# Performance work log

Measured on AMD Instinct MI355X. Metric: run time of the kernel, lower is better.

The kernel has to match this reference:

```python
import jax, jax.numpy as jnp
import numpy as np

N = 100000       # num nodes
E = 1000000      # num edges
D_IN = 128       # node_input_dim
H = 128          # hidden_dim
D_E = 32         # edge_input_dim
C = 16           # num_classes


def setup_inputs() -> dict:
    key = jax.random.key(0)
    ks = jax.random.split(key, 8)
    x = jax.random.normal(ks[0], (N, D_IN), dtype=jnp.float32)
    edge_index = jax.random.randint(ks[1], (2, E), 0, N)
    edge_attr = jax.random.normal(ks[2], (E, D_E), dtype=jnp.float32)

    def glorot(k, shape):
        fan = shape[0]
        return (jax.random.normal(k, shape, dtype=jnp.float32) / np.sqrt(fan)).astype(jnp.float32)

    W1 = glorot(ks[3], (D_IN, H)); b1 = jnp.zeros((H,), jnp.float32)
    W2 = glorot(ks[4], (H, H));    b2 = jnp.zeros((H,), jnp.float32)
    W3 = glorot(ks[5], (H, H));    b3 = jnp.zeros((H,), jnp.float32)
    W_fc = glorot(ks[6], (D_E + 2 * H, C)); b_fc = jnp.zeros((C,), jnp.float32)
    return {"x": x, "edge_index": edge_index, "edge_attr": edge_attr,
            "W1": W1, "b1": b1, "W2": W2, "b2": b2, "W3": W3, "b3": b3,
            "W_fc": W_fc, "b_fc": b_fc}


def gcn_conv(h_in, W, b, src, dst, dinv):
    """PyG GCNConv: h = D^-1/2 (A+I) D^-1/2 (h_in @ W) + b.
    Self-loop contribution handled analytically as dinv[i]^2 * h[i]."""
    h = h_in @ W                                      # [N, H]
    norm = dinv[src] * dinv[dst]                      # [E]
    msgs = h[src] * norm[:, None]                     # gather + scale, [E, H]
    agg = jax.ops.segment_sum(msgs, dst, num_segments=N)  # scatter-add
    agg = agg + h * (dinv * dinv)[:, None]            # self-loops
    return agg + b


def reference(x, edge_index, edge_attr, W1, b1, W2, b2, W3, b3, W_fc, b_fc):
    src, dst = edge_index[0], edge_index[1]
    # degree with self-loops (edge_weight = 1), as in PyG gcn_norm
    deg = jax.ops.segment_sum(jnp.ones((E,), jnp.float32), dst, num_segments=N) + 1.0
    dinv = jax.lax.rsqrt(deg)

    h = jax.nn.relu(gcn_conv(x, W1, b1, src, dst, dinv))
    # dropout(p=0.3) is identity in eval mode
    h = jax.nn.relu(gcn_conv(h, W2, b2, src, dst, dinv))
    h = jax.nn.relu(gcn_conv(h, W3, b3, src, dst, dinv))

    edge_features = jnp.concatenate([h[src], h[dst], edge_attr], axis=1)  # [E, 2H+D_E]
    edge_output = edge_features @ W_fc + b_fc                             # [E, C]
    return jax.nn.log_softmax(edge_output, axis=1)
```

## Files before the change

kernel.cpp:

```cpp
#include <hip/hip_runtime.h>
#include <hip/hip_bf16.h>

#define D_IN 128
#define HDIM 128
#define D_E  32
#define NC   16
#define SCAN_CHUNK 2048

typedef __attribute__((ext_vector_type(8))) short short8;
typedef __attribute__((ext_vector_type(4))) float float4v;

__device__ inline short f2bs(float f) {
  __hip_bfloat16 h = (__hip_bfloat16)f;
  return *reinterpret_cast<short*>(&h);
}

__device__ inline float bs2f(short s) {
  unsigned int u = ((unsigned int)(unsigned short)s) << 16;
  float f;
  __builtin_memcpy(&f, &u, 4);
  return f;
}


__global__ __launch_bounds__(256) void count_deg(const int* __restrict__ ei, int* __restrict__ deg, int E) {
  int e = blockIdx.x * 256 + threadIdx.x;
  if (e < E) atomicAdd(&deg[ei[E + e]], 1);
}

__global__ __launch_bounds__(256) void scan_blocksums(const int* __restrict__ deg, int* __restrict__ bsum, int n) {
  __shared__ int red[256];
  int t = threadIdx.x;
  int base = blockIdx.x * SCAN_CHUNK + t * 8;
  int s = 0;
#pragma unroll
  for (int j = 0; j < 8; ++j) {
    int i = base + j;
    if (i < n) s += deg[i];
  }
  red[t] = s;
  __syncthreads();
  for (int off = 128; off > 0; off >>= 1) {
    if (t < off) red[t] += red[t + off];
    __syncthreads();
  }
  if (t == 0) bsum[blockIdx.x] = red[0];
}

__global__ __launch_bounds__(256) void scan_offsets(const int* __restrict__ bsum, int* __restrict__ boff, int nb) {
  __shared__ int s[256];
  int t = threadIdx.x;
  int v = (t < nb) ? bsum[t] : 0;
  s[t] = v;
  __syncthreads();
  for (int off = 1; off < 256; off <<= 1) {
    int u = (t >= off) ? s[t - off] : 0;
    __syncthreads();
    s[t] += u;
    __syncthreads();
  }
  if (t < nb) boff[t] = (t == 0) ? 0 : s[t - 1];
}

__global__ __launch_bounds__(256) void scan_write(const int* __restrict__ deg, const int* __restrict__ boff,
                                                  int* __restrict__ rowptr, float* __restrict__ dinv, int n) {
  __shared__ int red[256];
  int t = threadIdx.x;
  int base = blockIdx.x * SCAN_CHUNK + t * 8;
  int v[8];
  int s = 0;
#pragma unroll
  for (int j = 0; j < 8; ++j) {
    int i = base + j;
    v[j] = (i < n) ? deg[i] : 0;
    s += v[j];
  }
  red[t] = s;
  __syncthreads();
  for (int off = 1; off < 256; off <<= 1) {
    int u = (t >= off) ? red[t - off] : 0;
    __syncthreads();
    red[t] += u;
    __syncthreads();
  }
  int run = red[t] - s + boff[blockIdx.x];
#pragma unroll
  for (int j = 0; j < 8; ++j) {
    int i = base + j;
    if (i < n) {
      rowptr[i] = run;
      dinv[i] = rsqrtf((float)v[j] + 1.0f);
    }
    run += v[j];
  }
}

__global__ __launch_bounds__(256) void fill_csr(const int* __restrict__ ei, const int* __restrict__ rowptr,
                                                int* __restrict__ cursor, int* __restrict__ col, int E) {
  int e = blockIdx.x * 256 + threadIdx.x;
  if (e < E) {
    int d = ei[E + e];
    int pos = atomicAdd(&cursor[d], 1);
    col[rowptr[d] + pos] = ei[e];
  }
}

__global__ __launch_bounds__(256) void repack_w128(const float* __restrict__ W, short* __restrict__ wp) {
  int idx = blockIdx.x * 256 + threadIdx.x;
  if (idx < 16384) {
    int j = idx & 7, lane = (idx >> 3) & 63, t = (idx >> 9) & 7, kc = idx >> 12;
    int k = kc * 32 + (lane >> 4) * 8 + j;
    int nn = t * 16 + (lane & 15);
    wp[idx] = f2bs(W[k * HDIM + nn]);
  }
}

__global__ __launch_bounds__(256) void repack_wcp(const float* __restrict__ Wfc, short* __restrict__ wp) {
  int idx = blockIdx.x * 256 + threadIdx.x;
  if (idx < 4096) {
    int j = idx & 7, lane = (idx >> 3) & 63, t = (idx >> 9) & 1, kc = idx >> 10;
    int k = kc * 32 + (lane >> 4) * 8 + j;
    int nn = t * 16 + (lane & 15);
    float v = (nn < 16) ? Wfc[k * NC + nn] : Wfc[(HDIM + k) * NC + (nn - 16)];
    wp[idx] = f2bs(v);
  }
}

template<int NCOL, bool FP32IN, bool FP32OUT, bool SCALE>
__global__ __launch_bounds__(256) void gemm_mfma(const void* __restrict__ Xv, const short* __restrict__ wpack,
                                                 void* __restrict__ Yv, const float* __restrict__ dscale, int n) {
  constexpr int NT = NCOL / 16;
  __shared__ short sw[4 * NT * 512];
  int tid = threadIdx.x;
  {
    const float4* wg = (const float4*)wpack;
    float4* sg = (float4*)sw;
    for (int i = tid; i < 4 * NT * 512 / 8; i += 256) sg[i] = wg[i];
  }
  __syncthreads();
  int wave = tid >> 6, lane = tid & 63;
  int quad = lane >> 4;
  int row = blockIdx.x * 64 + wave * 16 + (lane & 15);
  bool rowok = row < n;
  float4v acc[NT];
#pragma unroll
  for (int t = 0; t < NT; ++t) acc[t] = (float4v){0.f, 0.f, 0.f, 0.f};

#pragma unroll
  for (int kc = 0; kc < 4; ++kc) {
    short8 af = {0, 0, 0, 0, 0, 0, 0, 0};
    if (rowok) {
      if (FP32IN) {
        const float* xp = (const float*)Xv + (size_t)row * 128 + kc * 32 + quad * 8;
        float4 x0 = *(const float4*)xp;
        float4 x1 = *(const float4*)(xp + 4);
        af[0] = f2bs(x0.x); af[1] = f2bs(x0.y); af[2] = f2bs(x0.z); af[3] = f2bs(x0.w);
        af[4] = f2bs(x1.x); af[5] = f2bs(x1.y); af[6] = f2bs(x1.z); af[7] = f2bs(x1.w);
      } else {
        af = *(const short8*)((const short*)Xv + (size_t)row * 128 + kc * 32 + quad * 8);
      }
    }
#pragma unroll
    for (int t = 0; t < NT; ++t) {
      short8 bfr = *(const short8*)(sw + (kc * NT + t) * 512 + lane * 8);
      acc[t] = __builtin_amdgcn_mfma_f32_16x16x32_bf16(af, bfr, acc[t], 0, 0, 0);
    }
  }
  int orow0 = blockIdx.x * 64 + wave * 16 + quad * 4;
  float dv[4] = {1.f, 1.f, 1.f, 1.f};
  if constexpr (SCALE) {
#pragma unroll
    for (int r = 0; r < 4; ++r) dv[r] = (orow0 + r < n) ? dscale[orow0 + r] : 0.f;
  }
#pragma unroll
  for (int t = 0; t < NT; ++t) {
    int ocol = t * 16 + (lane & 15);
#pragma unroll
    for (int r = 0; r < 4; ++r) {
      int orow = orow0 + r;
      if (orow < n) {
        float val = acc[t][r];
        if constexpr (SCALE) val *= dv[r];
        if (FP32OUT)
          ((float*)Yv)[(size_t)orow * NCOL + ocol] = val;
        else
          ((__hip_bfloat16*)Yv)[(size_t)orow * NCOL + ocol] = (__hip_bfloat16)val;
      }
    }
  }
}

__global__ __launch_bounds__(256) void agg_vec(const __hip_bfloat16* __restrict__ hs, const float* __restrict__ dinv,
                                               const int* __restrict__ rowptr, const int* __restrict__ deg,
                                               const int* __restrict__ col, const float* __restrict__ bias,
                                               __hip_bfloat16* __restrict__ hout, int N) {
  int tid = threadIdx.x;
  int wave = tid >> 6, lane = tid & 63;
  int q = lane >> 4, ft = lane & 15;
  int i = blockIdx.x * 16 + wave * 4 + q;
  bool ok = i < N;
  int iS = ok ? i : (N - 1);
  int s0 = rowptr[iS];
  int dg = ok ? deg[iS] : 0;
  float di = dinv[iS];
  const short* hb = (const short*)hs;
  short8 selfv = *(const short8*)(hb + (size_t)iS * 128 + ft * 8);
  float acc[8];
#pragma unroll
  for (int j = 0; j < 8; ++j) acc[j] = bs2f(selfv[j]);
  int mx = dg;
  mx = max(mx, __shfl_xor(mx, 16));
  mx = max(mx, __shfl_xor(mx, 32));
  int cA = 0, cB = 0;
  if (0 < dg) cA = col[s0];
  if (1 < dg) cB = col[s0 + 1];
  for (int it = 0; it < mx; it += 2) {
    int nA = 0, nB = 0;
    if (it + 2 < dg) nA = col[s0 + it + 2];
    if (it + 3 < dg) nB = col[s0 + it + 3];
    if (it < dg) {
      short8 r0 = *(const short8*)(hb + (size_t)cA * 128 + ft * 8);
#pragma unroll
      for (int j = 0; j < 8; ++j) acc[j] += bs2f(r0[j]);
    }
    if (it + 1 < dg) {
      short8 r1 = *(const short8*)(hb + (size_t)cB * 128 + ft * 8);
#pragma unroll
      for (int j = 0; j < 8; ++j) acc[j] += bs2f(r1[j]);
    }
    cA = nA; cB = nB;
  }
  if (ok) {
    float4 b0 = *(const float4*)(bias + ft * 8);
    float4 b1 = *(const float4*)(bias + ft * 8 + 4);
    float bb[8] = {b0.x, b0.y, b0.z, b0.w, b1.x, b1.y, b1.z, b1.w};
    short8 o;
#pragma unroll
    for (int j = 0; j < 8; ++j) {
      float v = fmaxf(fmaf(acc[j], di, bb[j]), 0.f);
      o[j] = f2bs(v);
    }
    *(short8*)((short*)hout + (size_t)i * 128 + ft * 8) = o;
  }
}

__global__ __launch_bounds__(256) void edge_kernel(const int* __restrict__ ei, const float* __restrict__ ea,
                                                   const float* __restrict__ PQ, const float* __restrict__ Wfc,
                                                   const float* __restrict__ bfc, float* __restrict__ out, int E) {
  __shared__ float swe[D_E * NC];
  __shared__ float sb[NC];
  __shared__ float sea[256 * (D_E + 1)];
  int tid = threadIdx.x;
  int e0 = blockIdx.x * 256;
  for (int i = tid; i < D_E * NC; i += 256) {
    int j = i / NC, c = i % NC;
    swe[i] = Wfc[(2 * HDIM + j) * NC + c];
  }
  if (tid < NC) sb[tid] = bfc[tid];
  for (int i = tid; i < 256 * (D_E / 4); i += 256) {
    int le = i / (D_E / 4), f = i % (D_E / 4);
    int ge = e0 + le;
    float4 v = make_float4(0.f, 0.f, 0.f, 0.f);
    if (ge < E) v = *(const float4*)(ea + (size_t)ge * D_E + f * 4);
    float* p = sea + le * (D_E + 1) + f * 4;
    p[0] = v.x; p[1] = v.y; p[2] = v.z; p[3] = v.w;
  }
  __syncthreads();

  int e = e0 + tid;
  int s = 0, d = 0;
  if (e < E) { s = ei[e]; d = ei[E + e]; }
  float l[NC];
  {
    const float* p1 = PQ + (size_t)s * 32;
    const float* p2 = PQ + (size_t)d * 32 + 16;
#pragma unroll
    for (int c = 0; c < NC; ++c) l[c] = p1[c] + p2[c] + sb[c];
  }
  const float* myea = sea + tid * (D_E + 1);
#pragma unroll
  for (int j = 0; j < D_E; ++j) {
    float a = myea[j];
#pragma unroll
    for (int c = 0; c < NC; ++c) l[c] = fmaf(a, swe[j * NC + c], l[c]);
  }
  float m = l[0];
#pragma unroll
  for (int c = 1; c < NC; ++c) m = fmaxf(m, l[c]);
  float sum = 0.f;
#pragma unroll
  for (int c = 0; c < NC; ++c) sum += __expf(l[c] - m);
  float lse = __logf(sum) + m;
  if (e < E) {
    float4* po = (float4*)(out + (size_t)e * NC);
    po[0] = make_float4(l[0] - lse, l[1] - lse, l[2] - lse, l[3] - lse);
    po[1] = make_float4(l[4] - lse, l[5] - lse, l[6] - lse, l[7] - lse);
    po[2] = make_float4(l[8] - lse, l[9] - lse, l[10] - lse, l[11] - lse);
    po[3] = make_float4(l[12] - lse, l[13] - lse, l[14] - lse, l[15] - lse);
  }
}


extern "C" void kernel_launch(void* const* d_in, const int* in_sizes, int n_in,
                              void* d_out, int out_size, void* d_ws, size_t ws_size,
                              hipStream_t stream) {
  const float* x   = (const float*)d_in[0];
  const int*   ei  = (const int*)d_in[1];
  const float* ea  = (const float*)d_in[2];
  const float* W1  = (const float*)d_in[3];
  const float* b1  = (const float*)d_in[4];
  const float* W2  = (const float*)d_in[5];
  const float* b2  = (const float*)d_in[6];
  const float* W3  = (const float*)d_in[7];
  const float* b3  = (const float*)d_in[8];
  const float* Wfc = (const float*)d_in[9];
  const float* bfc = (const float*)d_in[10];
  float* out = (float*)d_out;
  int N = in_sizes[0] / D_IN;
  int E = in_sizes[1] / 2;

  char* w = (char*)d_ws;
  size_t off = 0;
  auto alloc = [&](size_t bytes) -> char* {
    char* p = w + off;
    off += (bytes + 255) & ~(size_t)255;
    return p;
  };
  __hip_bfloat16* A = (__hip_bfloat16*)alloc((size_t)N * HDIM * 2);
  __hip_bfloat16* B = (__hip_bfloat16*)alloc((size_t)N * HDIM * 2);
  float* PQ     = (float*)alloc((size_t)N * 32 * 4);
  int*   col    = (int*)alloc((size_t)E * 4);
  int*   deg    = (int*)alloc((size_t)N * 4);
  int*   cursor = (int*)alloc((size_t)N * 4);
  float* dinv   = (float*)alloc((size_t)N * 4);
  int*   rowptr = (int*)alloc((size_t)N * 4);
  int*   bsum   = (int*)alloc(1024 * 4);
  int*   boff   = (int*)alloc(1024 * 4);
  short* wp1    = (short*)alloc(16384 * 2);
  short* wp2    = (short*)alloc(16384 * 2);
  short* wp3    = (short*)alloc(16384 * 2);
  short* wpc    = (short*)alloc(4096 * 2);

  hipMemsetAsync(deg, 0, (size_t)N * 4, stream);
  hipMemsetAsync(cursor, 0, (size_t)N * 4, stream);

  int eb = (E + 255) / 256;
  int sb = (N + SCAN_CHUNK - 1) / SCAN_CHUNK;
  count_deg<<<eb, 256, 0, stream>>>(ei, deg, E);
  scan_blocksums<<<sb, 256, 0, stream>>>(deg, bsum, N);
  scan_offsets<<<1, 256, 0, stream>>>(bsum, boff, sb);
  scan_write<<<sb, 256, 0, stream>>>(deg, boff, rowptr, dinv, N);
  fill_csr<<<eb, 256, 0, stream>>>(ei, rowptr, cursor, col, E);
  repack_w128<<<64, 256, 0, stream>>>(W1, wp1);
  repack_w128<<<64, 256, 0, stream>>>(W2, wp2);
  repack_w128<<<64, 256, 0, stream>>>(W3, wp3);
  repack_wcp<<<16, 256, 0, stream>>>(Wfc, wpc);

  int gb = (N + 63) / 64;
  int ab = (N + 15) / 16;
  gemm_mfma<128, true,  false, true ><<<gb, 256, 0, stream>>>(x, wp1, A, dinv, N);
  agg_vec<<<ab, 256, 0, stream>>>(A, dinv, rowptr, deg, col, b1, B, N);
  gemm_mfma<128, false, false, true ><<<gb, 256, 0, stream>>>(B, wp2, A, dinv, N);
  agg_vec<<<ab, 256, 0, stream>>>(A, dinv, rowptr, deg, col, b2, B, N);
  gemm_mfma<128, false, false, true ><<<gb, 256, 0, stream>>>(B, wp3, A, dinv, N);
  agg_vec<<<ab, 256, 0, stream>>>(A, dinv, rowptr, deg, col, b3, B, N);
  gemm_mfma<32,  false, true,  false><<<gb, 256, 0, stream>>>(B, wpc, PQ, nullptr, N);
  edge_kernel<<<eb, 256, 0, stream>>>(ei, ea, PQ, Wfc, bfc, out, E);
}
```

Baseline: 610.9 us.

## Move edge-attr projection to MFMA pre-pass and deepen aggregation prefetch

Adds a separate MFMA kernel that projects edge attributes through the edge-feature slice of the classifier weight, adds the bias, and stores a bf16 [E,16] buffer. The edge kernel then only gathers node logits, adds this buffer and applies log-softmax, which removes the per-thread scalar 32x16 FMA loop and its shared-memory staging. In exchange it writes and re-reads an extra E×16 bf16 array and introduces bf16 rounding on the edge term. The aggregation loop also goes from two to four neighbour gathers per iteration to raise memory-level parallelism.

```diff
diff --git a/kernel.cpp b/kernel.cpp
--- a/kernel.cpp
+++ b/kernel.cpp
@@ -123,6 +123,16 @@
     int nn = t * 16 + (lane & 15);
     float v = (nn < 16) ? Wfc[k * NC + nn] : Wfc[(HDIM + k) * NC + (nn - 16)];
     wp[idx] = f2bs(v);
+  }
+}
+
+__global__ __launch_bounds__(256) void repack_wea(const float* __restrict__ Wfc, short* __restrict__ wp) {
+  int idx = blockIdx.x * 256 + threadIdx.x;
+  if (idx < 512) {
+    int j = idx & 7, lane = (idx >> 3) & 63;
+    int k = (lane >> 4) * 8 + j;
+    int nn = lane & 15;
+    wp[idx] = f2bs(Wfc[(2 * HDIM + k) * NC + nn]);
   }
 }
 
@@ -187,6 +197,37 @@
           ((__hip_bfloat16*)Yv)[(size_t)orow * NCOL + ocol] = (__hip_bfloat16)val;
       }
     }
+  }
+}
+
+__global__ __launch_bounds__(256) void gemm_ea(const float* __restrict__ ea, const short* __restrict__ wp,
+                                               const float* __restrict__ bfc, __hip_bfloat16* __restrict__ EA, int E) {
+  __shared__ short sw[512];
+  __shared__ float sb[16];
+  int tid = threadIdx.x;
+  if (tid < 64) ((float4*)sw)[tid] = ((const float4*)wp)[tid];
+  if (tid < 16) sb[tid] = bfc[tid];
+  __syncthreads();
+  int wave = tid >> 6, lane = tid & 63, quad = lane >> 4;
+  int row = blockIdx.x * 64 + wave * 16 + (lane & 15);
+  short8 af = {0, 0, 0, 0, 0, 0, 0, 0};
+  if (row < E) {
+    const float* xp = ea + (size_t)row * D_E + quad * 8;
+    float4 x0 = *(const float4*)xp;
+    float4 x1 = *(const float4*)(xp + 4);
+    af[0] = f2bs(x0.x); af[1] = f2bs(x0.y); af[2] = f2bs(x0.z); af[3] = f2bs(x0.w);
+    af[4] = f2bs(x1.x); af[5] = f2bs(x1.y); af[6] = f2bs(x1.z); af[7] = f2bs(x1.w);
+  }
+  short8 bfr = *(const short8*)(sw + lane * 8);
+  float4v acc = (float4v){0.f, 0.f, 0.f, 0.f};
+  acc = __builtin_amdgcn_mfma_f32_16x16x32_bf16(af, bfr, acc, 0, 0, 0);
+  int orow0 = blockIdx.x * 64 + wave * 16 + quad * 4;
+  int ocol = lane & 15;
+  float bb = sb[ocol];
+#pragma unroll
+  for (int r = 0; r < 4; ++r) {
+    int orow = orow0 + r;
+    if (orow < E) EA[(size_t)orow * NC + ocol] = (__hip_bfloat16)(acc[r] + bb);
   }
 }
 
@@ -211,13 +252,17 @@
   int mx = dg;
   mx = max(mx, __shfl_xor(mx, 16));
   mx = max(mx, __shfl_xor(mx, 32));
-  int cA = 0, cB = 0;
+  int cA = 0, cB = 0, cC = 0, cD = 0;
   if (0 < dg) cA = col[s0];
   if (1 < dg) cB = col[s0 + 1];
-  for (int it = 0; it < mx; it += 2) {
-    int nA = 0, nB = 0;
-    if (it + 2 < dg) nA = col[s0 + it + 2];
-    if (it + 3 < dg) nB = col[s0 + it + 3];
+  if (2 < dg) cC = col[s0 + 2];
+  if (3 < dg) cD = col[s0 + 3];
+  for (int it = 0; it < mx; it += 4) {
+    int nA = 0, nB = 0, nC = 0, nD = 0;
+    if (it + 4 < dg) nA = col[s0 + it + 4];
+    if (it + 5 < dg) nB = col[s0 + it + 5];
+    if (it + 6 < dg) nC = col[s0 + it + 6];
+    if (it + 7 < dg) nD = col[s0 + it + 7];
     if (it < dg) {
       short8 r0 = *(const short8*)(hb + (size_t)cA * 128 + ft * 8);
 #pragma unroll
@@ -228,7 +273,17 @@
 #pragma unroll
       for (int j = 0; j < 8; ++j) acc[j] += bs2f(r1[j]);
     }
-    cA = nA; cB = nB;
+    if (it + 2 < dg) {
+      short8 r2 = *(const short8*)(hb + (size_t)cC * 128 + ft * 8);
+#pragma unroll
+      for (int j = 0; j < 8; ++j) acc[j] += bs2f(r2[j]);
+    }
+    if (it + 3 < dg) {
+      short8 r3 = *(const short8*)(hb + (size_t)cD * 128 + ft * 8);
+#pragma unroll
+      for (int j = 0; j < 8; ++j) acc[j] += bs2f(r3[j]);
+    }
+    cA = nA; cB = nB; cC = nC; cD = nD;
   }
   if (ok) {
     float4 b0 = *(const float4*)(bias + ft * 8);
@@ -244,46 +299,36 @@
   }
 }
 
-__global__ __launch_bounds__(256) void edge_kernel(const int* __restrict__ ei, const float* __restrict__ ea,
-                                                   const float* __restrict__ PQ, const float* __restrict__ Wfc,
-                                                   const float* __restrict__ bfc, float* __restrict__ out, int E) {
-  __shared__ float swe[D_E * NC];
-  __shared__ float sb[NC];
-  __shared__ float sea[256 * (D_E + 1)];
-  int tid = threadIdx.x;
-  int e0 = blockIdx.x * 256;
-  for (int i = tid; i < D_E * NC; i += 256) {
-    int j = i / NC, c = i % NC;
-    swe[i] = Wfc[(2 * HDIM + j) * NC + c];
-  }
-  if (tid < NC) sb[tid] = bfc[tid];
-  for (int i = tid; i < 256 * (D_E / 4); i += 256) {
-    int le = i / (D_E / 4), f = i % (D_E / 4);
-    int ge = e0 + le;
-    float4 v = make_float4(0.f, 0.f, 0.f, 0.f);
-    if (ge < E) v = *(const float4*)(ea + (size_t)ge * D_E + f * 4);
-    float* p = sea + le * (D_E + 1) + f * 4;
-    p[0] = v.x; p[1] = v.y; p[2] = v.z; p[3] = v.w;
-  }
-  __syncthreads();
-
-  int e = e0 + tid;
-  int s = 0, d = 0;
-  if (e < E) { s = ei[e]; d = ei[E + e]; }
+__global__ __launch_bounds__(256) void edge_final(const int* __restrict__ ei, const __hip_bfloat16* __restrict__ EA,
+                                                  const float* __restrict__ PQ, float* __restrict__ out, int E) {
+  int e = blockIdx.x * 256 + threadIdx.x;
+  bool ok = e < E;
+  int ec = ok ? e : (E - 1);
+  int s = ei[ec], d = ei[E + ec];
+  const float4* p1 = (const float4*)(PQ + (size_t)s * 32);
+  const float4* p2 = (const float4*)(PQ + (size_t)d * 32 + 16);
+  const short* eb = (const short*)EA + (size_t)ec * NC;
+  short8 ev0 = *(const short8*)eb;
+  short8 ev1 = *(const short8*)(eb + 8);
   float l[NC];
-  {
-    const float* p1 = PQ + (size_t)s * 32;
-    const float* p2 = PQ + (size_t)d * 32 + 16;
-#pragma unroll
-    for (int c = 0; c < NC; ++c) l[c] = p1[c] + p2[c] + sb[c];
-  }
-  const float* myea = sea + tid * (D_E + 1);
-#pragma unroll
-  for (int j = 0; j < D_E; ++j) {
-    float a = myea[j];
-#pragma unroll
-    for (int c = 0; c < NC; ++c) l[c] = fmaf(a, swe[j * NC + c], l[c]);
-  }
+  float4 P0 = p1[0], P1 = p1[1], P2 = p1[2], P3 = p1[3];
+  float4 Q0 = p2[0], Q1 = p2[1], Q2 = p2[2], Q3 = p2[3];
+  l[0]  = P0.x + Q0.x + bs2f(ev0[0]);
+  l[1]  = P0.y + Q0.y + bs2f(ev0[1]);
+  l[2]  = P0.z + Q0.z + bs2f(ev0[2]);
+  l[3]  = P0.w + Q0.w + bs2f(ev0[3]);
+  l[4]  = P1.x + Q1.x + bs2f(ev0[4]);
+  l[5]  = P1.y + Q1.y + bs2f(ev0[5]);
+  l[6]  = P1.z + Q1.z + bs2f(ev0[6]);
+  l[7]  = P1.w + Q1.w + bs2f(ev0[7]);
+  l[8]  = P2.x + Q2.x + bs2f(ev1[0]);
+  l[9]  = P2.y + Q2.y + bs2f(ev1[1]);
+  l[10] = P2.z + Q2.z + bs2f(ev1[2]);
+  l[11] = P2.w + Q2.w + bs2f(ev1[3]);
+  l[12] = P3.x + Q3.x + bs2f(ev1[4]);
+  l[13] = P3.y + Q3.y + bs2f(ev1[5]);
+  l[14] = P3.z + Q3.z + bs2f(ev1[6]);
+  l[15] = P3.w + Q3.w + bs2f(ev1[7]);
   float m = l[0];
 #pragma unroll
   for (int c = 1; c < NC; ++c) m = fmaxf(m, l[c]);
@@ -291,7 +336,7 @@
 #pragma unroll
   for (int c = 0; c < NC; ++c) sum += __expf(l[c] - m);
   float lse = __logf(sum) + m;
-  if (e < E) {
+  if (ok) {
     float4* po = (float4*)(out + (size_t)e * NC);
     po[0] = make_float4(l[0] - lse, l[1] - lse, l[2] - lse, l[3] - lse);
     po[1] = make_float4(l[4] - lse, l[5] - lse, l[6] - lse, l[7] - lse);
@@ -329,6 +374,7 @@
   __hip_bfloat16* A = (__hip_bfloat16*)alloc((size_t)N * HDIM * 2);
   __hip_bfloat16* B = (__hip_bfloat16*)alloc((size_t)N * HDIM * 2);
   float* PQ     = (float*)alloc((size_t)N * 32 * 4);
+  __hip_bfloat16* EA = (__hip_bfloat16*)alloc((size_t)E * NC * 2);
   int*   col    = (int*)alloc((size_t)E * 4);
   int*   deg    = (int*)alloc((size_t)N * 4);
   int*   cursor = (int*)alloc((size_t)N * 4);
@@ -340,6 +386,7 @@
   short* wp2    = (short*)alloc(16384 * 2);
   short* wp3    = (short*)alloc(16384 * 2);
   short* wpc    = (short*)alloc(4096 * 2);
+  short* wpe    = (short*)alloc(512 * 2);
 
   hipMemsetAsync(deg, 0, (size_t)N * 4, stream);
   hipMemsetAsync(cursor, 0, (size_t)N * 4, stream);
@@ -355,9 +402,12 @@
   repack_w128<<<64, 256, 0, stream>>>(W2, wp2);
   repack_w128<<<64, 256, 0, stream>>>(W3, wp3);
   repack_wcp<<<16, 256, 0, stream>>>(Wfc, wpc);
+  repack_wea<<<2, 256, 0, stream>>>(Wfc, wpe);
 
   int gb = (N + 63) / 64;
   int ab = (N + 15) / 16;
+  int geb = (E + 63) / 64;
+  gemm_ea<<<geb, 256, 0, stream>>>(ea, wpe, bfc, EA, E);
   gemm_mfma<128, true,  false, true ><<<gb, 256, 0, stream>>>(x, wp1, A, dinv, N);
   agg_vec<<<ab, 256, 0, stream>>>(A, dinv, rowptr, deg, col, b1, B, N);
   gemm_mfma<128, false, false, true ><<<gb, 256, 0, stream>>>(B, wp2, A, dinv, N);
@@ -365,5 +415,5 @@
   gemm_mfma<128, false, false, true ><<<gb, 256, 0, stream>>>(B, wp3, A, dinv, N);
   agg_vec<<<ab, 256, 0, stream>>>(A, dinv, rowptr, deg, col, b3, B, N);
   gemm_mfma<32,  false, true,  false><<<gb, 256, 0, stream>>>(B, wpc, PQ, nullptr, N);
-  edge_kernel<<<eb, 256, 0, stream>>>(ei, ea, PQ, Wfc, bfc, out, E);
-}
+  edge_final<<<eb, 256, 0, stream>>>(ei, EA, PQ, out, E);
+}
```

Result: no change. 620.4 us (+1.6%).
